# Kernel tuning notes

Hardware: AMD Instinct MI355X
Metric: run time of the kernel (lower is better)

Reference implementation:

```python
import jax, jax.numpy as jnp
import numpy as np


def setup_inputs() -> dict:
    key = jax.random.key(0)
    k1, k2, k3, k4, k5 = jax.random.split(key, 5)
    B, S, E, H, D = 8, 1024, 1024, 8, 128  # batch, seq, embed, heads, hidden/head
    stdv = 1.0 / np.sqrt(D)
    return {
        "k": jax.random.normal(k1, (B, S, E), jnp.float32),
        "q": jax.random.normal(k2, (B, S, E), jnp.float32),
        "flag": 0,  # False: project q through w_qx
        "w_kx": jax.random.uniform(k3, (H, E, D), jnp.float32, -stdv, stdv),
        "w_qx": jax.random.uniform(k4, (H, E, D), jnp.float32, -stdv, stdv),
        "proj_w": jax.random.normal(k5, (E, H * D), jnp.float32) * 0.02,  # out_dim = embed_dim
        "proj_b": jnp.zeros((E,), jnp.float32),
    }


def reference(k, q, flag, w_kx, w_qx, proj_w, proj_b):
    H, E, D = w_kx.shape
    B, Sk, _ = k.shape
    Sq = q.shape[1]
    # per-head tanh projections: [H, B, S, D]
    kx = jnp.tanh(jnp.einsum("bse,hed->hbsd", k, w_kx))
    if flag:
        qx = jnp.broadcast_to(q[None], (H,) + q.shape)  # q already in hidden space
    else:
        qx = jnp.tanh(jnp.einsum("bse,hed->hbsd", q, w_qx))
    # scaled dot product scores [H, B, Sq, Sk]
    score = jnp.einsum("hbqd,hbkd->hbqk", qx, kx) / jnp.sqrt(jnp.float32(D))
    attn = jax.nn.softmax(score, axis=-1)
    out = jnp.einsum("hbqk,hbkd->hbqd", attn, kx)  # [H, B, Sq, D]
    # concat heads: [B, Sq, H*D], then output projection (dropout p=0 is identity)
    out = jnp.transpose(out, (1, 2, 0, 3)).reshape(B, Sq, H * D)
    return out @ proj_w.T + proj_b
```

## Files before the change

### kernel.cpp

```cpp
#include <hip/hip_runtime.h>

typedef unsigned short u16;
typedef unsigned int u32;
typedef __bf16 bf16x8 __attribute__((ext_vector_type(8)));
typedef float f32x4 __attribute__((ext_vector_type(4)));

#define MFMA16(a, b, c) __builtin_amdgcn_mfma_f32_16x16x32_bf16(a, b, c, 0, 0, 0)
#define EXP2(x) __builtin_amdgcn_exp2f(x)

typedef const void __attribute__((address_space(1)))* gas1_t;
typedef void __attribute__((address_space(3)))* las3_t;

__device__ __forceinline__ void gload16(const void* g, void* l) {
  __builtin_amdgcn_global_load_lds((gas1_t)g, (las3_t)l, 16, 0, 0);
}

__device__ __forceinline__ u16 f2bf(float f) {
  union { float f; u32 u; } v; v.f = f;
  u32 r = v.u + 0x7FFFu + ((v.u >> 16) & 1u);
  return (u16)(r >> 16);
}

__device__ __forceinline__ float fast_tanh(float x) {
  float xc = fminf(fmaxf(x, -20.f), 20.f);
  float t = EXP2(xc * 2.885390081777927f);
  return (t - 1.0f) * __builtin_amdgcn_rcpf(t + 1.0f);
}

__global__ __launch_bounds__(256) void cvt_kernel(const float* __restrict__ in,
                                                  u16* __restrict__ out, int n8) {
  int i = blockIdx.x * blockDim.x + threadIdx.x;
  int stride = gridDim.x * blockDim.x;
  for (; i < n8; i += stride) {
    const float4* p = (const float4*)(in + (size_t)i * 8);
    float4 a = p[0], b = p[1];
    u16 t[8];
    t[0] = f2bf(a.x); t[1] = f2bf(a.y); t[2] = f2bf(a.z); t[3] = f2bf(a.w);
    t[4] = f2bf(b.x); t[5] = f2bf(b.y); t[6] = f2bf(b.z); t[7] = f2bf(b.w);
    *(uint4*)(out + (size_t)i * 8) = *(uint4*)t;
  }
}

__global__ __launch_bounds__(256) void wtrans_kernel(const float* __restrict__ w,
                                                     u16* __restrict__ wT) {
  __shared__ float t[64][65];
  int h = blockIdx.z;
  int e0 = blockIdx.x * 64, d0 = blockIdx.y * 64;
  const float* src = w + (size_t)h * 1024 * 128;
  u16* dst = wT + (size_t)h * 128 * 1024;
  int tid = threadIdx.x;
  {
    int row = tid >> 2, c0 = (tid & 3) * 16;
#pragma unroll
    for (int i = 0; i < 4; ++i) {
      float4 v = *(const float4*)(src + (size_t)(e0 + row) * 128 + d0 + c0 + i * 4);
      t[row][c0 + i * 4 + 0] = v.x;
      t[row][c0 + i * 4 + 1] = v.y;
      t[row][c0 + i * 4 + 2] = v.z;
      t[row][c0 + i * 4 + 3] = v.w;
    }
  }
  __syncthreads();
  {
    int dl = tid >> 2, c0 = (tid & 3) * 16;
    u16 tmp[16];
#pragma unroll
    for (int i = 0; i < 16; ++i) tmp[i] = f2bf(t[c0 + i][dl]);
    u16* o = dst + (size_t)(d0 + dl) * 1024 + e0 + c0;
    *(uint4*)o = *(uint4*)tmp;
    *(uint4*)(o + 8) = *(uint4*)(tmp + 8);
  }
}

__device__ __forceinline__ void gemm_core128_db(const u16* Abase, const u16* Bbase,
                                                int K,
                                                u16* A0, u16* B0, u16* A1, u16* B1,
                                                f32x4 (&acc)[4][4]) {
  const int tid = threadIdx.x, lane = tid & 63, wid = tid >> 6;
  const int wr = wid >> 1, wc = wid & 1;
  const int nkt = K >> 6;

#define GSTAGE(Al, Bl, kt_)                                                     \
  do {                                                                          \
    _Pragma("unroll") for (int i_ = 0; i_ < 4; ++i_) {                          \
      int cIdx = (wid * 4 + i_) * 64 + lane;                                    \
      int row = cIdx >> 3, slot = cIdx & 7;                                     \
      int src = slot ^ (row & 7);                                               \
      gload16((const char*)Abase + ((size_t)row * K + (kt_) * 64 + src * 8) * 2,\
              (char*)(Al) + (wid * 4 + i_) * 1024);                             \
      gload16((const char*)Bbase + ((size_t)row * K + (kt_) * 64 + src * 8) * 2,\
              (char*)(Bl) + (wid * 4 + i_) * 1024);                             \
    }                                                                           \
  } while (0)

#define GCOMPUTE(Al, Bl)                                                        \
  do {                                                                          \
    __builtin_amdgcn_s_setprio(1);                                              \
    _Pragma("unroll") for (int kc = 0; kc < 2; ++kc) {                          \
      bf16x8 af[4], bb[4];                                                      \
      _Pragma("unroll") for (int f = 0; f < 4; ++f) {                           \
        int arow = wr * 64 + f * 16 + (lane & 15);                              \
        int ch = kc * 4 + (lane >> 4);                                          \
        af[f] = *(const bf16x8*)((Al) + arow * 64 + ((ch ^ (arow & 7)) << 3));  \
        int brow = wc * 64 + f * 16 + (lane & 15);                              \
        bb[f] = *(const bf16x8*)((Bl) + brow * 64 + ((ch ^ (brow & 7)) << 3));  \
      }                                                                         \
      _Pragma("unroll") for (int mf = 0; mf < 4; ++mf)                          \
        _Pragma("unroll") for (int nf = 0; nf < 4; ++nf)                        \
          acc[mf][nf] = MFMA16(af[mf], bb[nf], acc[mf][nf]);                    \
    }                                                                           \
    __builtin_amdgcn_s_setprio(0);                                              \
  } while (0)

  GSTAGE(A0, B0, 0);
  for (int it = 0; it < nkt / 2 - 1; ++it) {
    GSTAGE(A1, B1, 2 * it + 1);
    asm volatile("s_waitcnt vmcnt(8)" ::: "memory");
    __builtin_amdgcn_s_barrier();
    GCOMPUTE(A0, B0);
    __builtin_amdgcn_s_barrier();
    GSTAGE(A0, B0, 2 * it + 2);
    asm volatile("s_waitcnt vmcnt(8)" ::: "memory");
    __builtin_amdgcn_s_barrier();
    GCOMPUTE(A1, B1);
    __builtin_amdgcn_s_barrier();
  }
  GSTAGE(A1, B1, nkt - 1);
  asm volatile("s_waitcnt vmcnt(8)" ::: "memory");
  __builtin_amdgcn_s_barrier();
  GCOMPUTE(A0, B0);
  asm volatile("s_waitcnt vmcnt(0)" ::: "memory");
  __builtin_amdgcn_s_barrier();
  GCOMPUTE(A1, B1);
#undef GSTAGE
#undef GCOMPUTE
}

__global__ __launch_bounds__(256) void gemm_tanh_kernel(
    const u16* __restrict__ Ak, const u16* __restrict__ Aq,
    const u16* __restrict__ wTk, const u16* __restrict__ wTq,
    u16* __restrict__ kxo, u16* __restrict__ qxo) {
  __shared__ alignas(16) u16 A0[128 * 64], B0[128 * 64];
  __shared__ alignas(16) u16 A1[128 * 64], B1[128 * 64];
  const u16* A; const u16* W; u16* C;
  if (blockIdx.z == 0) { A = Ak; W = wTk; C = kxo; }
  else { A = Aq; W = wTq; C = qxo; }
  int h = blockIdx.y;
  int mBase = blockIdx.x * 128;
  f32x4 acc[4][4];
#pragma unroll
  for (int i = 0; i < 4; ++i)
#pragma unroll
    for (int j = 0; j < 4; ++j) acc[i][j] = (f32x4){0.f, 0.f, 0.f, 0.f};
  gemm_core128_db(A + (size_t)mBase * 1024, W + (size_t)h * 128 * 1024, 1024,
                  A0, B0, A1, B1, acc);
  const int lane = threadIdx.x & 63, wid = threadIdx.x >> 6;
  const int wr = wid >> 1, wc = wid & 1;
  u16* Ch = C + (size_t)h * 8192 * 128;
#pragma unroll
  for (int mf = 0; mf < 4; ++mf)
#pragma unroll
    for (int nf = 0; nf < 4; ++nf)
#pragma unroll
      for (int j = 0; j < 4; ++j) {
        int m = mBase + wr * 64 + mf * 16 + ((lane >> 4) << 2) + j;
        int d = wc * 64 + nf * 16 + (lane & 15);
        Ch[(size_t)m * 128 + d] = f2bf(fast_tanh(acc[mf][nf][j]));
      }
}

__global__ __launch_bounds__(256) void transpose_kernel(const u16* __restrict__ kx,
                                                        u16* __restrict__ kxT) {
  __shared__ u16 t[64][72];
  int hb = blockIdx.z;
  const u16* src = kx + (size_t)hb * 1024 * 128;
  u16* dst = kxT + (size_t)hb * 128 * 1024;
  int s0 = blockIdx.x * 64, d0 = blockIdx.y * 64;
  int tid = threadIdx.x;
#pragma unroll
  for (int r = 0; r < 2; ++r) {
    int row = r * 32 + (tid >> 3), c8 = (tid & 7) * 8;
    uint4 v = *(const uint4*)(src + (size_t)(s0 + row) * 128 + d0 + c8);
    *(uint4*)&t[row][c8] = v;
  }
  __syncthreads();
#pragma unroll
  for (int r = 0; r < 2; ++r) {
    int dl = r * 32 + (tid >> 3), s8 = (tid & 7) * 8;
    u16 tmp[8];
#pragma unroll
    for (int i = 0; i < 8; ++i) tmp[i] = t[s8 + i][dl];
    *(uint4*)(dst + (size_t)(d0 + dl) * 1024 + s0 + s8) = *(uint4*)tmp;
  }
}

__global__ __launch_bounds__(256, 2) void attn_kernel(const u16* __restrict__ qx,
                                                      const u16* __restrict__ kx,
                                                      const u16* __restrict__ kxT,
                                                      u16* __restrict__ X) {
  __shared__ alignas(16) u16 Klds[2][64 * 128];
  __shared__ alignas(16) u16 Vlds[2][128 * 64];
  __shared__ alignas(16) u16 Plds[4][32 * 64];
  const int tid = threadIdx.x, lane = tid & 63, wid = tid >> 6;
  const int g = lane >> 4, l15 = lane & 15;
  const int hb = blockIdx.x, qt = blockIdx.y, h = hb >> 3, b = hb & 7;
  const u16* qxh = qx + ((size_t)h * 8192 + (size_t)b * 1024) * 128;
  const u16* kxh = kx + ((size_t)h * 8192 + (size_t)b * 1024) * 128;
  const u16* kxTh = kxT + (size_t)hb * 128 * 1024;
  const int q0 = qt * 128 + wid * 32;
  const float SC = 0.08838834764831845f * 1.44269504088896340f;

#define STAGE(buf, kt_)                                                        \
  do {                                                                         \
    _Pragma("unroll") for (int i_ = 0; i_ < 4; ++i_) {                         \
      int cIdx = (wid * 4 + i_) * 64 + lane;                                   \
      {                                                                        \
        int row = cIdx >> 4, slot = cIdx & 15;                                 \
        int src = slot ^ (row & 7);                                            \
        gload16((const char*)kxh + (size_t)((kt_) * 64 + row) * 256 + src * 16,\
                (char*)&Klds[buf][0] + (wid * 4 + i_) * 1024);                 \
      }                                                                        \
      {                                                                        \
        int row = cIdx >> 3, slot = cIdx & 7;                                  \
        int src = slot ^ (row & 7);                                            \
        gload16((const char*)kxTh + (size_t)row * 2048 + (kt_) * 128 + src * 16,\
                (char*)&Vlds[buf][0] + (wid * 4 + i_) * 1024);                 \
      }                                                                        \
    }                                                                          \
  } while (0)

  bf16x8 qa[2][4];
#pragma unroll
  for (int m = 0; m < 2; ++m)
#pragma unroll
    for (int kc = 0; kc < 4; ++kc)
      qa[m][kc] = *(const bf16x8*)(qxh + (size_t)(q0 + m * 16 + l15) * 128
                                   + kc * 32 + g * 8);

  f32x4 os[2][8];
#pragma unroll
  for (int i = 0; i < 2; ++i)
#pragma unroll
    for (int j = 0; j < 8; ++j) os[i][j] = (f32x4){0.f, 0.f, 0.f, 0.f};
  float lsum[2] = {0.f, 0.f};

  u16* Pw = &Plds[wid][0];

  STAGE(0, 0);

  for (int kt = 0; kt < 16; ++kt) {
    const int cur = kt & 1;
    if (kt < 15) {
      STAGE(cur ^ 1, kt + 1);
      asm volatile("s_waitcnt vmcnt(8)" ::: "memory");
    } else {
      asm volatile("s_waitcnt vmcnt(0)" ::: "memory");
    }
    __builtin_amdgcn_s_barrier();

    const u16* Kc = &Klds[cur][0];
    const u16* Vc = &Vlds[cur][0];

    f32x4 sa[4][2];
#pragma unroll
    for (int i = 0; i < 4; ++i)
#pragma unroll
      for (int j = 0; j < 2; ++j) sa[i][j] = (f32x4){0.f, 0.f, 0.f, 0.f};
    __builtin_amdgcn_s_setprio(1);
#pragma unroll
    for (int kc = 0; kc < 4; ++kc) {
      bf16x8 kb[4];
#pragma unroll
      for (int t = 0; t < 4; ++t) {
        int row = t * 16 + l15;
        int ch = kc * 4 + g;
        kb[t] = *(const bf16x8*)(Kc + row * 128 + ((ch ^ (row & 7)) << 3));
      }
#pragma unroll
      for (int t = 0; t < 4; ++t)
#pragma unroll
        for (int m = 0; m < 2; ++m)
          sa[t][m] = MFMA16(kb[t], qa[m][kc], sa[t][m]);
    }
    __builtin_amdgcn_s_setprio(0);

#pragma unroll
    for (int m = 0; m < 2; ++m) {
      int q = m * 16 + l15;
      int rowb = q * 128, q7 = q & 7;
#pragma unroll
      for (int t = 0; t < 4; ++t) {
        float p0 = EXP2(sa[t][m][0] * SC);
        float p1 = EXP2(sa[t][m][1] * SC);
        float p2 = EXP2(sa[t][m][2] * SC);
        float p3 = EXP2(sa[t][m][3] * SC);
        lsum[m] += (p0 + p1) + (p2 + p3);
        uint2 pk;
        pk.x = (u32)f2bf(p0) | ((u32)f2bf(p1) << 16);
        pk.y = (u32)f2bf(p2) | ((u32)f2bf(p3) << 16);
        int slot = (2 * t + (g >> 1)) ^ q7;
        *(uint2*)((char*)Pw + rowb + slot * 16 + 8 * (g & 1)) = pk;
      }
    }

    __builtin_amdgcn_s_setprio(1);
#pragma unroll
    for (int kc2 = 0; kc2 < 2; ++kc2) {
      bf16x8 pa[2], vb[8];
#pragma unroll
      for (int m = 0; m < 2; ++m) {
        int q = m * 16 + l15;
        int slot = (g + 4 * kc2) ^ (q & 7);
        pa[m] = *(const bf16x8*)((char*)Pw + q * 128 + slot * 16);
      }
#pragma unroll
      for (int nd = 0; nd < 8; ++nd) {
        int row = nd * 16 + l15;
        int ch = kc2 * 4 + g;
        vb[nd] = *(const bf16x8*)(Vc + row * 64 + ((ch ^ (row & 7)) << 3));
      }
#pragma unroll
      for (int m = 0; m < 2; ++m)
#pragma unroll
        for (int nd = 0; nd < 8; ++nd)
          os[m][nd] = MFMA16(pa[m], vb[nd], os[m][nd]);
    }
    __builtin_amdgcn_s_setprio(0);
    __builtin_amdgcn_s_barrier();
  }
#undef STAGE

#pragma unroll
  for (int m = 0; m < 2; ++m) {
    float s = lsum[m];
    s += __shfl_xor(s, 16);
    s += __shfl_xor(s, 32);
    lsum[m] = s;
  }

#pragma unroll
  for (int m = 0; m < 2; ++m)
#pragma unroll
    for (int j = 0; j < 4; ++j) {
      float tot = __shfl(lsum[m], 4 * g + j, 64);
      float inv = 1.f / tot;
      int qrow = b * 1024 + q0 + m * 16 + g * 4 + j;
#pragma unroll
      for (int nd = 0; nd < 8; ++nd) {
        int col = h * 128 + nd * 16 + l15;
        X[(size_t)qrow * 1024 + col] = f2bf(os[m][nd][j] * inv);
      }
    }
}

__global__ __launch_bounds__(256) void gemm_bias_kernel(
    const u16* __restrict__ X, const u16* __restrict__ pw,
    const float* __restrict__ pb, float* __restrict__ out) {
  __shared__ alignas(16) u16 A0[128 * 64], B0[128 * 64];
  __shared__ alignas(16) u16 A1[128 * 64], B1[128 * 64];
  int mBase = blockIdx.x * 128;
  int nBase = blockIdx.y * 128;
  f32x4 acc[4][4];
#pragma unroll
  for (int i = 0; i < 4; ++i)
#pragma unroll
    for (int j = 0; j < 4; ++j) acc[i][j] = (f32x4){0.f, 0.f, 0.f, 0.f};
  gemm_core128_db(X + (size_t)mBase * 1024, pw + (size_t)nBase * 1024, 1024,
                  A0, B0, A1, B1, acc);
  const int lane = threadIdx.x & 63, wid = threadIdx.x >> 6;
  const int wr = wid >> 1, wc = wid & 1;
#pragma unroll
  for (int nf = 0; nf < 4; ++nf) {
    int e = nBase + wc * 64 + nf * 16 + (lane & 15);
    float bv = pb[e];
#pragma unroll
    for (int mf = 0; mf < 4; ++mf)
#pragma unroll
      for (int j = 0; j < 4; ++j) {
        int m = mBase + wr * 64 + mf * 16 + ((lane >> 4) << 2) + j;
        out[(size_t)m * 1024 + e] = acc[mf][nf][j] + bv;
      }
  }
}

extern "C" void kernel_launch(void* const* d_in, const int* in_sizes, int n_in,
                              void* d_out, int out_size, void* d_ws, size_t ws_size,
                              hipStream_t stream) {
  const float* k = (const float*)d_in[0];
  const float* q = (const float*)d_in[1];
  const float* wk = (const float*)d_in[3];
  const float* wq = (const float*)d_in[4];
  const float* pw = (const float*)d_in[5];
  const float* pb = (const float*)d_in[6];
  float* out = (float*)d_out;
  char* ws = (char*)d_ws;

  u16* kbf = (u16*)(ws);
  u16* qbf = (u16*)(ws + (16ull << 20));
  u16* wTk = (u16*)(ws + (32ull << 20));
  u16* wTq = (u16*)(ws + (34ull << 20));
  u16* pwb = (u16*)(ws + (36ull << 20));
  u16* kx  = (u16*)(ws + (38ull << 20));
  u16* qx  = (u16*)(ws + (54ull << 20));
  u16* kxT = (u16*)(ws + (70ull << 20));
  u16* X   = kbf;

  cvt_kernel<<<2048, 256, 0, stream>>>(k, kbf, 1048576);
  cvt_kernel<<<2048, 256, 0, stream>>>(q, qbf, 1048576);
  cvt_kernel<<<512, 256, 0, stream>>>(pw, pwb, 131072);
  wtrans_kernel<<<dim3(16, 2, 8), 256, 0, stream>>>(wk, wTk);
  wtrans_kernel<<<dim3(16, 2, 8), 256, 0, stream>>>(wq, wTq);
  gemm_tanh_kernel<<<dim3(64, 8, 2), 256, 0, stream>>>(kbf, qbf, wTk, wTq, kx, qx);
  transpose_kernel<<<dim3(16, 2, 64), 256, 0, stream>>>(kx, kxT);
  attn_kernel<<<dim3(64, 8), 256, 0, stream>>>(qx, kx, kxT, X);
  gemm_bias_kernel<<<dim3(64, 8), 256, 0, stream>>>(X, pwb, pb, out);
}
```

Measured before the change: 141.0 us.

## Fuse fp32-to-bf16 conversion of k and q into the tanh projection GEMM

Drops the two standalone conversion kernels for k and q. The projection GEMM now loads fp32 activations straight into registers, rounds them to bf16 and writes them into swizzled LDS, while B still uses async global-to-LDS loads with a rewritten double-buffered loop and launch bounds of 2 blocks per CU. This removes a full fp32 read plus bf16 write and re-read of both 32MB inputs. In exchange each of the 8 head blocks re-reads the A tile as fp32, doubling A traffic into the GEMM, and adds register pressure and conversion ALU work in the main loop.

```diff
diff --git a/kernel.cpp b/kernel.cpp
--- a/kernel.cpp
+++ b/kernel.cpp
@@ -70,6 +70,128 @@
     *(uint4*)o = *(uint4*)tmp;
     *(uint4*)(o + 8) = *(uint4*)(tmp + 8);
   }
+}
+
+__device__ __forceinline__ void gemm_core128_f32A(const float* __restrict__ Af,
+                                                  const u16* __restrict__ Bbase,
+                                                  int K,
+                                                  u16* A0, u16* B0, u16* A1, u16* B1,
+                                                  f32x4 (&acc)[4][4]) {
+  const int tid = threadIdx.x, lane = tid & 63, wid = tid >> 6;
+  const int wr = wid >> 1, wc = wid & 1;
+  const int nkt = K >> 6;
+  int crow[4], csrc[4], coff[4];
+#pragma unroll
+  for (int i = 0; i < 4; ++i) {
+    int c = (wid * 4 + i) * 64 + lane;
+    crow[i] = c >> 3;
+    int slot = c & 7;
+    csrc[i] = slot ^ (crow[i] & 7);
+    coff[i] = c * 16;
+  }
+  float4 fa[4][2];
+
+#define ISSUEA(kt_)                                                             \
+  _Pragma("unroll") for (int i_ = 0; i_ < 4; ++i_) {                            \
+    const float* p_ = Af + (size_t)crow[i_] * K + (kt_) * 64 + csrc[i_] * 8;    \
+    fa[i_][0] = *(const float4*)p_;                                             \
+    fa[i_][1] = *(const float4*)(p_ + 4);                                       \
+  }
+#define WRITEA(Al)                                                              \
+  _Pragma("unroll") for (int i_ = 0; i_ < 4; ++i_) {                            \
+    u16 t_[8];                                                                  \
+    t_[0] = f2bf(fa[i_][0].x); t_[1] = f2bf(fa[i_][0].y);                       \
+    t_[2] = f2bf(fa[i_][0].z); t_[3] = f2bf(fa[i_][0].w);                       \
+    t_[4] = f2bf(fa[i_][1].x); t_[5] = f2bf(fa[i_][1].y);                       \
+    t_[6] = f2bf(fa[i_][1].z); t_[7] = f2bf(fa[i_][1].w);                       \
+    *(uint4*)((char*)(Al) + coff[i_]) = *(uint4*)t_;                            \
+  }
+#define GLOADB(Bl, kt_)                                                         \
+  _Pragma("unroll") for (int i_ = 0; i_ < 4; ++i_) {                            \
+    gload16((const char*)Bbase + ((size_t)crow[i_] * K + (kt_) * 64             \
+                                  + csrc[i_] * 8) * 2,                          \
+            (char*)(Bl) + (wid * 4 + i_) * 1024);                               \
+  }
+#define CMP128(Al, Bl)                                                          \
+  do {                                                                          \
+    __builtin_amdgcn_s_setprio(1);                                              \
+    _Pragma("unroll") for (int kc = 0; kc < 2; ++kc) {                          \
+      bf16x8 af[4], bb[4];                                                      \
+      _Pragma("unroll") for (int f = 0; f < 4; ++f) {                           \
+        int arow = wr * 64 + f * 16 + (lane & 15);                              \
+        int ch = kc * 4 + (lane >> 4);                                          \
+        af[f] = *(const bf16x8*)((Al) + arow * 64 + ((ch ^ (arow & 7)) << 3));  \
+        int brow = wc * 64 + f * 16 + (lane & 15);                              \
+        bb[f] = *(const bf16x8*)((Bl) + brow * 64 + ((ch ^ (brow & 7)) << 3));  \
+      }                                                                         \
+      _Pragma("unroll") for (int mf = 0; mf < 4; ++mf)                          \
+        _Pragma("unroll") for (int nf = 0; nf < 4; ++nf)                        \
+          acc[mf][nf] = MFMA16(af[mf], bb[nf], acc[mf][nf]);                    \
+    }                                                                           \
+    __builtin_amdgcn_s_setprio(0);                                              \
+  } while (0)
+
+  ISSUEA(0);
+  GLOADB(B0, 0);
+  asm volatile("s_waitcnt vmcnt(4)" ::: "memory");
+  WRITEA(A0);
+
+  for (int it = 0; it < nkt; ++it) {
+    const bool pf = (it + 1 < nkt);
+    u16* Acur = (it & 1) ? A1 : A0;
+    u16* Bcur = (it & 1) ? B1 : B0;
+    u16* Anxt = (it & 1) ? A0 : A1;
+    u16* Bnxt = (it & 1) ? B0 : B1;
+    if (pf) {
+      ISSUEA(it + 1);
+      GLOADB(Bnxt, it + 1);
+      asm volatile("s_waitcnt vmcnt(4)" ::: "memory");
+      WRITEA(Anxt);
+    } else {
+      asm volatile("s_waitcnt vmcnt(0)" ::: "memory");
+    }
+    asm volatile("s_waitcnt lgkmcnt(0)" ::: "memory");
+    __builtin_amdgcn_s_barrier();
+    CMP128(Acur, Bcur);
+    __builtin_amdgcn_s_barrier();
+  }
+#undef ISSUEA
+#undef WRITEA
+#undef GLOADB
+#undef CMP128
+}
+
+__global__ __launch_bounds__(256, 2) void gemm_tanh_kernel(
+    const float* __restrict__ Ak, const float* __restrict__ Aq,
+    const u16* __restrict__ wTk, const u16* __restrict__ wTq,
+    u16* __restrict__ kxo, u16* __restrict__ qxo) {
+  __shared__ alignas(16) u16 A0[128 * 64], B0[128 * 64];
+  __shared__ alignas(16) u16 A1[128 * 64], B1[128 * 64];
+  const float* A; const u16* W; u16* C;
+  if (blockIdx.z == 0) { A = Ak; W = wTk; C = kxo; }
+  else { A = Aq; W = wTq; C = qxo; }
+  int h = blockIdx.y;
+  int mBase = blockIdx.x * 128;
+  f32x4 acc[4][4];
+#pragma unroll
+  for (int i = 0; i < 4; ++i)
+#pragma unroll
+    for (int j = 0; j < 4; ++j) acc[i][j] = (f32x4){0.f, 0.f, 0.f, 0.f};
+  gemm_core128_f32A(A + (size_t)mBase * 1024, W + (size_t)h * 128 * 1024, 1024,
+                    A0, B0, A1, B1, acc);
+  const int lane = threadIdx.x & 63, wid = threadIdx.x >> 6;
+  const int wr = wid >> 1, wc = wid & 1;
+  u16* Ch = C + (size_t)h * 8192 * 128;
+#pragma unroll
+  for (int mf = 0; mf < 4; ++mf)
+#pragma unroll
+    for (int nf = 0; nf < 4; ++nf)
+#pragma unroll
+      for (int j = 0; j < 4; ++j) {
+        int m = mBase + wr * 64 + mf * 16 + ((lane >> 4) << 2) + j;
+        int d = wc * 64 + nf * 16 + (lane & 15);
+        Ch[(size_t)m * 128 + d] = f2bf(fast_tanh(acc[mf][nf][j]));
+      }
 }
 
 __device__ __forceinline__ void gemm_core128_db(const u16* Abase, const u16* Bbase,
@@ -136,39 +258,6 @@
 #undef GCOMPUTE
 }
 
-__global__ __launch_bounds__(256) void gemm_tanh_kernel(
-    const u16* __restrict__ Ak, const u16* __restrict__ Aq,
-    const u16* __restrict__ wTk, const u16* __restrict__ wTq,
-    u16* __restrict__ kxo, u16* __restrict__ qxo) {
-  __shared__ alignas(16) u16 A0[128 * 64], B0[128 * 64];
-  __shared__ alignas(16) u16 A1[128 * 64], B1[128 * 64];
-  const u16* A; const u16* W; u16* C;
-  if (blockIdx.z == 0) { A = Ak; W = wTk; C = kxo; }
-  else { A = Aq; W = wTq; C = qxo; }
-  int h = blockIdx.y;
-  int mBase = blockIdx.x * 128;
-  f32x4 acc[4][4];
-#pragma unroll
-  for (int i = 0; i < 4; ++i)
-#pragma unroll
-    for (int j = 0; j < 4; ++j) acc[i][j] = (f32x4){0.f, 0.f, 0.f, 0.f};
-  gemm_core128_db(A + (size_t)mBase * 1024, W + (size_t)h * 128 * 1024, 1024,
-                  A0, B0, A1, B1, acc);
-  const int lane = threadIdx.x & 63, wid = threadIdx.x >> 6;
-  const int wr = wid >> 1, wc = wid & 1;
-  u16* Ch = C + (size_t)h * 8192 * 128;
-#pragma unroll
-  for (int mf = 0; mf < 4; ++mf)
-#pragma unroll
-    for (int nf = 0; nf < 4; ++nf)
-#pragma unroll
-      for (int j = 0; j < 4; ++j) {
-        int m = mBase + wr * 64 + mf * 16 + ((lane >> 4) << 2) + j;
-        int d = wc * 64 + nf * 16 + (lane & 15);
-        Ch[(size_t)m * 128 + d] = f2bf(fast_tanh(acc[mf][nf][j]));
-      }
-}
-
 __global__ __launch_bounds__(256) void transpose_kernel(const u16* __restrict__ kx,
                                                         u16* __restrict__ kxT) {
   __shared__ u16 t[64][72];
@@ -395,22 +484,18 @@
   float* out = (float*)d_out;
   char* ws = (char*)d_ws;
 
-  u16* kbf = (u16*)(ws);
-  u16* qbf = (u16*)(ws + (16ull << 20));
+  u16* X   = (u16*)(ws);
   u16* wTk = (u16*)(ws + (32ull << 20));
   u16* wTq = (u16*)(ws + (34ull << 20));
   u16* pwb = (u16*)(ws + (36ull << 20));
   u16* kx  = (u16*)(ws + (38ull << 20));
   u16* qx  = (u16*)(ws + (54ull << 20));
   u16* kxT = (u16*)(ws + (70ull << 20));
-  u16* X   = kbf;
-
-  cvt_kernel<<<2048, 256, 0, stream>>>(k, kbf, 1048576);
-  cvt_kernel<<<2048, 256, 0, stream>>>(q, qbf, 1048576);
+
   cvt_kernel<<<512, 256, 0, stream>>>(pw, pwb, 131072);
   wtrans_kernel<<<dim3(16, 2, 8), 256, 0, stream>>>(wk, wTk);
   wtrans_kernel<<<dim3(16, 2, 8), 256, 0, stream>>>(wq, wTq);
-  gemm_tanh_kernel<<<dim3(64, 8, 2), 256, 0, stream>>>(kbf, qbf, wTk, wTq, kx, qx);
+  gemm_tanh_kernel<<<dim3(64, 8, 2), 256, 0, stream>>>(k, q, wTk, wTq, kx, qx);
   transpose_kernel<<<dim3(16, 2, 64), 256, 0, stream>>>(kx, kxT);
   attn_kernel<<<dim3(64, 8), 256, 0, stream>>>(qx, kx, kxT, X);
   gemm_bias_kernel<<<dim3(64, 8), 256, 0, stream>>>(X, pwb, pb, out);
```

Result: no change. 143.6 us (+1.8%).
